# Performance work log

Measured on AMD Instinct MI355X. Metric: run time of the kernel, lower is better.

The kernel has to match this reference:

```python
import jax, jax.numpy as jnp
import numpy as np

DECAY = 0.99
EPS = 1e-5  # Laplace smoothing eps in cluster-size balancing


def _quantize(z_flat, embedding, cluster_size, emb_avg, n_codes):
    # z_flat: [N, D]; embedding: [K, D]
    d = (jnp.sum(z_flat * z_flat, axis=1, keepdims=True)
         + jnp.sum(embedding * embedding, axis=1)
         - 2.0 * (z_flat @ embedding.T))                      # [N, K]
    idx = jnp.argmin(d, axis=1)                               # [N]
    # EMA update (training path). segment_sum == one-hot matmul scatter-add.
    counts = jax.ops.segment_sum(jnp.ones(z_flat.shape[0], z_flat.dtype), idx,
                                 num_segments=n_codes)        # [K]
    new_cs = cluster_size * DECAY + (1.0 - DECAY) * counts
    dw = jax.ops.segment_sum(z_flat, idx, num_segments=n_codes)  # [K, D]
    new_avg = emb_avg * DECAY + (1.0 - DECAY) * dw
    n = new_cs.sum()
    bal = (new_cs + EPS) / (n + n_codes * EPS) * n
    # torch assigns via .data (no autograd) -> stop_gradient for faithfulness
    new_emb = jax.lax.stop_gradient(new_avg / bal[:, None])
    z_q = jnp.take(new_emb, idx, axis=0)  # == one_hot(idx) @ new_emb
    return idx, z_q


def _l2norm(x):
    # F.normalize(x, dim=-1) with eps=1e-12
    return x / jnp.maximum(jnp.linalg.norm(x, axis=-1, keepdims=True), 1e-12)


def reference(z, structure_embedding, style_embedding,
              structure_cluster_size, style_cluster_size,
              structure_embedding_avg, style_embedding_avg):
    b, c, h, w, d = z.shape
    zp = jnp.transpose(z, (0, 2, 3, 4, 1))      # b h w d c
    z_flat = zp.reshape(-1, c)                  # [N, D]
    s_idx, s_q = _quantize(z_flat, structure_embedding, structure_cluster_size,
                           structure_embedding_avg, structure_embedding.shape[0])
    y_idx, y_q = _quantize(z_flat, style_embedding, style_cluster_size,
                           style_embedding_avg, style_embedding.shape[0])

    def back(q):  # [N, C] -> b c h w d
        return jnp.transpose(q.reshape(b, h, w, d, c), (0, 4, 1, 2, 3))

    s_enc = back(s_q)
    y_enc = back(y_q)
    # NOTE: faithful to source — normalize over LAST axis of (b,c,h,w,d),
    # i.e. the spatial depth axis, exactly as F.normalize(dim=-1) does there.
    dis = jnp.mean(jnp.sum(_l2norm(s_enc) * _l2norm(y_enc), axis=-1) ** 2)
    z_q = (s_enc + y_enc) * 0.5
    return z_q, dis, s_idx, y_idx


def setup_inputs() -> dict:
    key = jax.random.key(0)
    k1, k2, k3 = jax.random.split(key, 3)
    B, C, H, W, D = 16, 256, 16, 16, 16
    Ks, Ky = 1024, 512
    return {
        "z": jax.random.normal(k1, (B, C, H, W, D), dtype=jnp.float32),
        "structure_embedding": jax.random.normal(k2, (Ks, C), dtype=jnp.float32),
        "style_embedding": jax.random.normal(k3, (Ky, C), dtype=jnp.float32),
        "structure_cluster_size": jnp.zeros((Ks,), jnp.float32),
        "style_cluster_size": jnp.zeros((Ky,), jnp.float32),
        "structure_embedding_avg": jnp.zeros((Ks, C), jnp.float32),
        "style_embedding_avg": jnp.zeros((Ky, C), jnp.float32),
    }
```

## Files before the change

kernel.cpp:

```cpp
#include <hip/hip_runtime.h>
#include <float.h>

#define NROWS 65536
#define CDIM  256
#define KS    1024
#define KY    512
#define KTOT  1536
#define SPB   4096

#define WB_CNT_S       0
#define WB_CNT_Y       4096
#define WB_RESCUE_CNT  6144
#define WB_DISACC      6152
#define WB_DW_S        6400
#define WB_DW_Y        1054976
#define WB_ZERO_BYTES  1579264
#define WB_EIMG        1579264
#define WB_EN2         2365696
#define WB_IDXS_I      2371840
#define WB_IDXY_I      2633984
#define WB_RLIST_S     2896128
#define WB_RLIST_Y     3158272
#define WB_BASE_S      3420416
#define WB_BASE_Y      3424512
#define WB_CUR_S       3426560
#define WB_CUR_Y       3430656
#define WB_SCALE_S     3432704
#define WB_SCALE_Y     3436800
#define WB_PERM_S      3438848
#define WB_PERM_Y      3700992
#define WB_KSORT_S     3963136
#define WB_KSORT_Y     4225280
#define WB_PS0         4487424
#define WB_PS1         5011712

#define OFF_OUT_ZQ   0
#define OFF_OUT_DIS  16777216
#define OFF_OUT_SIDX 16777217
#define OFF_OUT_YIDX 16842753

typedef __attribute__((ext_vector_type(8)))  _Float16 f16x8;
typedef __attribute__((ext_vector_type(4)))  float    f32x4;

__device__ __forceinline__ unsigned int umn(unsigned int a, unsigned int b) { return a < b ? a : b; }
__device__ __forceinline__ unsigned int umx(unsigned int a, unsigned int b) { return a > b ? a : b; }

__global__ void prep_kernel(const float* __restrict__ Es, const float* __restrict__ Ey,
                            const float* __restrict__ z,
                            unsigned short* __restrict__ eimg, float* __restrict__ en2,
                            float* __restrict__ zf) {
    if (blockIdx.x < 384) {
        int wave = threadIdx.x >> 6, lane = threadIdx.x & 63;
        int k = blockIdx.x * 4 + wave;
        const float* E = (k < KS) ? (Es + (size_t)k * CDIM) : (Ey + (size_t)(k - KS) * CDIM);
        float4 v = *(const float4*)(E + lane * 4);
        float nrm = v.x * v.x + v.y * v.y + v.z * v.z + v.w * v.w;
#pragma unroll
        for (int off = 32; off > 0; off >>= 1) nrm += __shfl_down(nrm, off);
        if (lane == 0) en2[k] = nrm;

        unsigned short q0 = __builtin_bit_cast(unsigned short, (_Float16)v.x);
        unsigned short q1 = __builtin_bit_cast(unsigned short, (_Float16)v.y);
        unsigned short q2 = __builtin_bit_cast(unsigned short, (_Float16)v.z);
        unsigned short q3 = __builtin_bit_cast(unsigned short, (_Float16)v.w);
        uint2 hp = make_uint2((unsigned)q0 | ((unsigned)q1 << 16),
                              (unsigned)q2 | ((unsigned)q3 << 16));
        int c0 = lane * 4;
        int kc = c0 >> 5, g = (c0 >> 3) & 3, j0 = c0 & 7;
        size_t byteoff = (size_t)(k >> 4) * 8192 + (size_t)kc * 1024
                       + (size_t)(g * 16 + (k & 15)) * 16 + (size_t)j0 * 2;
        *(uint2*)((char*)eimg + byteoff) = hp;
    } else {
        __shared__ float Zs[32][257];
        int blk = blockIdx.x - 384;
        int n0 = blk * 32, b = n0 >> 12, s0 = n0 & 4095;
        int t = threadIdx.x;
        const float* zb = z + (size_t)b * CDIM * SPB + s0;
#pragma unroll
        for (int i = 0; i < 32; ++i) {
            int l = i * 256 + t;
            int c = l >> 5, s = l & 31;
            Zs[s][c] = zb[(size_t)c * SPB + s];
        }
        __syncthreads();
#pragma unroll
        for (int j = 0; j < 8; ++j) {
            int gid = j * 256 + t;
            int nl = gid >> 6, fg = gid & 63;
            float4 v = *(const float4*)(&Zs[nl][fg * 4]);
            *(float4*)(&zf[(size_t)(n0 + nl) * 256 + fg * 4]) = v;
        }
    }
}

__device__ __forceinline__ void stage1(const unsigned short* __restrict__ eimg,
                                       int chunk, char* lds, int wave, int lane) {
    const char* gs = (const char*)eimg + (size_t)chunk * 8192 + wave * 2048 + lane * 16;
    char* ls = lds + wave * 2048;
    __builtin_amdgcn_global_load_lds(
        (const __attribute__((address_space(1))) void*)gs,
        (__attribute__((address_space(3))) void*)ls, 16, 0, 0);
    __builtin_amdgcn_global_load_lds(
        (const __attribute__((address_space(1))) void*)(gs + 1024),
        (__attribute__((address_space(3))) void*)(ls + 1024), 16, 0, 0);
}

#define WAITV(n)                                                               \
    asm volatile("s_waitcnt vmcnt(" #n ")");                                   \
    __builtin_amdgcn_sched_barrier(0);

#define PSFLUSH(dst)                                                           \
    {                                                                          \
        _Pragma("unroll")                                                      \
        for (int rg = 0; rg < 2; ++rg)                                         \
        _Pragma("unroll")                                                      \
        for (int q = 0; q < 4; ++q) {                                          \
            unsigned int v1 = m1a[rg][q], v2 = m2a[rg][q];                     \
            _Pragma("unroll")                                                  \
            for (int m = 8; m >= 1; m >>= 1) {                                 \
                unsigned int o1 = (unsigned int)__shfl_xor((int)v1, m);        \
                unsigned int o2 = (unsigned int)__shfl_xor((int)v2, m);        \
                v2 = umn(umn(v2, o2), umx(v1, o1));                            \
                v1 = umn(v1, o1);                                              \
            }                                                                  \
            if ((lane & 15) == 0) {                                            \
                int n = n0 + rg * 16 + (lane >> 4) * 4 + q;                    \
                dst[n] = make_uint2(v1, v2);                                   \
            }                                                                  \
            m1a[rg][q] = 0xFFFFFFFFu; m2a[rg][q] = 0xFFFFFFFFu;                \
        }                                                                      \
    }

#define FLUSHY()                                                               \
    {                                                                          \
        _Pragma("unroll")                                                      \
        for (int rg = 0; rg < 2; ++rg)                                         \
        _Pragma("unroll")                                                      \
        for (int q = 0; q < 4; ++q) {                                          \
            unsigned int v1 = m1a[rg][q], v2 = m2a[rg][q];                     \
            _Pragma("unroll")                                                  \
            for (int m = 8; m >= 1; m >>= 1) {                                 \
                unsigned int o1 = (unsigned int)__shfl_xor((int)v1, m);        \
                unsigned int o2 = (unsigned int)__shfl_xor((int)v2, m);        \
                v2 = umn(umn(v2, o2), umx(v1, o1));                            \
                v1 = umn(v1, o1);                                              \
            }                                                                  \
            if ((lane & 15) == 0) {                                            \
                int kw = (int)(v1 & 0x7FFu) - KS;                              \
                int n = n0 + rg * 16 + (lane >> 4) * 4 + q;                    \
                yidx_f[n] = (float)kw;                                         \
                yidx_i[n] = kw;                                                \
                atomicAdd(&cnt_y[kw], 1);                                      \
                if ((v1 >> 11) + 4 > (v2 >> 11)) {                             \
                    int k2w = (int)(v2 & 0x7FFu) - KS;                         \
                    int pp = atomicAdd(&rescue_cnt[1], 1);                     \
                    if (pp < 65536) rlist_y[pp] = n | (k2w << 16);             \
                }                                                              \
            }                                                                  \
        }                                                                      \
    }

__launch_bounds__(256, 4)
__global__ void assign_kernel(const float* __restrict__ zf, const unsigned short* __restrict__ eimg,
                              const float* __restrict__ en2g,
                              uint2* __restrict__ ps0, uint2* __restrict__ ps1,
                              float* __restrict__ yidx_f, int* __restrict__ yidx_i,
                              int* __restrict__ cnt_y, int* __restrict__ rescue_cnt,
                              int* __restrict__ rlist_y) {
    __shared__ char  sh[4][8192];
    __shared__ float en2l[KTOT];
    const int tid = threadIdx.x, wave = tid >> 6, lane = tid & 63;
    const int half = blockIdx.x & 1;
    const int n0 = (blockIdx.x >> 1) * 128 + wave * 32;
    const int cb = half * 48;

    for (int i = tid; i < KTOT; i += 256) en2l[i] = en2g[i];

    f16x8 A[2][8];
#pragma unroll
    for (int rg = 0; rg < 2; ++rg) {
        const float* zr = zf + (size_t)(n0 + rg * 16 + (lane & 15)) * 256 + (lane >> 4) * 8;
#pragma unroll
        for (int kc = 0; kc < 8; ++kc) {
            float4 f0 = *(const float4*)(zr + kc * 32);
            float4 f1 = *(const float4*)(zr + kc * 32 + 4);
            f16x8 a;
            a[0] = (_Float16)f0.x; a[1] = (_Float16)f0.y;
            a[2] = (_Float16)f0.z; a[3] = (_Float16)f0.w;
            a[4] = (_Float16)f1.x; a[5] = (_Float16)f1.y;
            a[6] = (_Float16)f1.z; a[7] = (_Float16)f1.w;
            A[rg][kc] = a;
        }
    }

    unsigned int m1a[2][4], m2a[2][4];
#pragma unroll
    for (int rg = 0; rg < 2; ++rg)
#pragma unroll
        for (int q = 0; q < 4; ++q) { m1a[rg][q] = 0xFFFFFFFFu; m2a[rg][q] = 0xFFFFFFFFu; }

    stage1(eimg, cb + 0, &sh[0][0], wave, lane);
    stage1(eimg, cb + 1, &sh[1][0], wave, lane);
    stage1(eimg, cb + 2, &sh[2][0], wave, lane);
    __syncthreads();

#pragma unroll 1
    for (int i = 0; i < 48; ++i) {
        if (i < 46)       { WAITV(4); }
        else if (i == 46) { WAITV(2); }
        else              { WAITV(0); }
        __builtin_amdgcn_s_barrier();
        asm volatile("" ::: "memory");
        if (i + 3 < 48) stage1(eimg, cb + i + 3, &sh[(i + 3) & 3][0], wave, lane);

        const int chunk = cb + i;
        const char* bb = &sh[i & 3][0] + lane * 16;
        f32x4 acc0 = {}, acc1 = {};
#pragma unroll
        for (int kc = 0; kc < 8; ++kc) {
            f16x8 B = *(const f16x8*)(bb + kc * 1024);
            acc0 = __builtin_amdgcn_mfma_f32_16x16x32_f16(A[0][kc], B, acc0, 0, 0, 0);
            acc1 = __builtin_amdgcn_mfma_f32_16x16x32_f16(A[1][kc], B, acc1, 0, 0, 0);
        }
        const int kcode = chunk * 16 + (lane & 15);
        const float en0 = en2l[kcode] + 512.0f;
        const unsigned int tag = (unsigned int)kcode;
#pragma unroll
        for (int q = 0; q < 4; ++q) {
            float d0 = fmaf(-2.f, acc0[q], en0);
            unsigned int du0 = (__float_as_uint(d0) & 0xFFFFF800u) | tag;
            m2a[0][q] = umn(m2a[0][q], umx(m1a[0][q], du0));
            m1a[0][q] = umn(m1a[0][q], du0);
            float d1 = fmaf(-2.f, acc1[q], en0);
            unsigned int du1 = (__float_as_uint(d1) & 0xFFFFF800u) | tag;
            m2a[1][q] = umn(m2a[1][q], umx(m1a[1][q], du1));
            m1a[1][q] = umn(m1a[1][q], du1);
        }

        if (half == 1 && i == 15) PSFLUSH(ps1);
    }

    if (half == 0) { PSFLUSH(ps0); }
    else           { FLUSHY(); }
}

__global__ void merge_s_kernel(const uint2* __restrict__ ps0, const uint2* __restrict__ ps1,
                               float* __restrict__ sidx_f, int* __restrict__ sidx_i,
                               int* __restrict__ cnt_s, int* __restrict__ rescue_cnt,
                               int* __restrict__ rlist_s) {
    int n = blockIdx.x * 256 + threadIdx.x;
    uint2 a = ps0[n], b = ps1[n];
    unsigned int v1 = umn(a.x, b.x);
    unsigned int v2 = umn(umn(a.y, b.y), umx(a.x, b.x));
    int kw = (int)(v1 & 0x7FFu);
    sidx_f[n] = (float)kw;
    sidx_i[n] = kw;
    atomicAdd(&cnt_s[kw], 1);
    if ((v1 >> 11) + 4 > (v2 >> 11)) {
        int k2w = (int)(v2 & 0x7FFu);
        int pp = atomicAdd(&rescue_cnt[0], 1);
        if (pp < 65536) rlist_s[pp] = n | (k2w << 16);
    }
}

__global__ void rescue2_kernel(const float* __restrict__ zf,
                               const float* __restrict__ Es, const float* __restrict__ Ey,
                               const float* __restrict__ en2, const int* __restrict__ rcnt,
                               const int* __restrict__ rlist_s, const int* __restrict__ rlist_y,
                               float* __restrict__ sidx_f, float* __restrict__ yidx_f,
                               int* __restrict__ sidx_i, int* __restrict__ yidx_i,
                               int* __restrict__ cnt_s, int* __restrict__ cnt_y) {
    int cs = rcnt[0]; if (cs > 65536) cs = 65536;
    int cy = rcnt[1]; if (cy > 65536) cy = 65536;
    int total = cs + cy;
    const int lane = threadIdx.x & 63;
    const int nw = (gridDim.x * blockDim.x) >> 6;
    for (int e = (int)((blockIdx.x * blockDim.x + threadIdx.x) >> 6); e < total; e += nw) {
        int book = (e >= cs);
        unsigned int ent = (unsigned int)(book ? rlist_y[e - cs] : rlist_s[e]);
        int n  = (int)(ent & 0xFFFFu);
        int k2 = (int)(ent >> 16);
        int* idx_i = book ? yidx_i : sidx_i;
        float* idx_f = book ? yidx_f : sidx_f;
        int* cnt = book ? cnt_y : cnt_s;
        const float* E = book ? Ey : Es;
        const float* en2k = book ? (en2 + KS) : en2;
        int k1 = idx_i[n];
        float4 zv = *(const float4*)(zf + (size_t)n * 256 + lane * 4);
        float4 a  = *(const float4*)(E + (size_t)k1 * 256 + lane * 4);
        float4 c  = *(const float4*)(E + (size_t)k2 * 256 + lane * 4);
        float d1 = zv.x * a.x + zv.y * a.y + zv.z * a.z + zv.w * a.w;
        float d2 = zv.x * c.x + zv.y * c.y + zv.z * c.z + zv.w * c.w;
#pragma unroll
        for (int off = 32; off > 0; off >>= 1) {
            d1 += __shfl_down(d1, off);
            d2 += __shfl_down(d2, off);
        }
        if (lane == 0) {
            float dist1 = en2k[k1] - 2.f * d1;
            float dist2 = en2k[k2] - 2.f * d2;
            int nk = (dist2 < dist1 || (dist2 == dist1 && k2 < k1)) ? k2 : k1;
            if (nk != k1) {
                atomicSub(&cnt[k1], 1);
                atomicAdd(&cnt[nk], 1);
                idx_i[n] = nk;
                idx_f[n] = (float)nk;
            }
        }
    }
}

__global__ void scanbal_kernel(const float* __restrict__ cs_in, const float* __restrict__ cy_in,
                               const int* __restrict__ cnt_s, const int* __restrict__ cnt_y,
                               int* __restrict__ base_s, int* __restrict__ base_y,
                               int* __restrict__ cur_s, int* __restrict__ cur_y,
                               float* __restrict__ scale_s, float* __restrict__ scale_y) {
    __shared__ int   sc[1024];
    __shared__ float sf[1024];
    int K = blockIdx.x ? KY : KS;
    const float* csi = blockIdx.x ? cy_in : cs_in;
    const int*   cnt = blockIdx.x ? cnt_y : cnt_s;
    int* base = blockIdx.x ? base_y : base_s;
    int* cur  = blockIdx.x ? cur_y  : cur_s;
    float* scale = blockIdx.x ? scale_y : scale_s;
    int t = threadIdx.x;
    int c = (t < K) ? cnt[t] : 0;
    float ncs = (t < K) ? (csi[t] * 0.99f + 0.01f * (float)c) : 0.f;
    sc[t] = c;
    __syncthreads();
    for (int off = 1; off < 1024; off <<= 1) {
        int v = sc[t] + ((t >= off) ? sc[t - off] : 0);
        __syncthreads();
        sc[t] = v;
        __syncthreads();
    }
    int incl = sc[t];
    sf[t] = ncs;
    __syncthreads();
    for (int s2 = 512; s2 > 0; s2 >>= 1) {
        if (t < s2) sf[t] += sf[t + s2];
        __syncthreads();
    }
    float nsum = sf[0];
    if (t < K) {
        base[t] = incl - c;
        cur[t]  = incl - c;
        float bal = (ncs + 1e-5f) / (nsum + (float)K * 1e-5f) * nsum;
        scale[t] = 1.0f / bal;
    }
}

__global__ void scatter_kernel(const int* __restrict__ si, const int* __restrict__ yi,
                               int* __restrict__ cur_s, int* __restrict__ cur_y,
                               int* __restrict__ perm_s, int* __restrict__ perm_y,
                               int* __restrict__ ksort_s, int* __restrict__ ksort_y) {
    int i = blockIdx.x * 256 + threadIdx.x;
    if (i < NROWS) {
        int k = si[i]; int p = atomicAdd(&cur_s[k], 1);
        perm_s[p] = i; ksort_s[p] = k;
    } else {
        int n = i - NROWS; int k = yi[n]; int p = atomicAdd(&cur_y[k], 1);
        perm_y[p] = n; ksort_y[p] = k;
    }
}

__global__ void dw_kernel(const float* __restrict__ zf,
                          const int* __restrict__ perm_s, const int* __restrict__ ksort_s,
                          const int* __restrict__ perm_y, const int* __restrict__ ksort_y,
                          float* __restrict__ dw_s, float* __restrict__ dw_y) {
    __shared__ int keys[65];
    __shared__ int rows[64];
    const int t = threadIdx.x;
    int blk = blockIdx.x;
    const int* perm; const int* ks; float* dw; int p0;
    if (blk < NROWS / 64) { perm = perm_s; ks = ksort_s; dw = dw_s; p0 = blk * 64; }
    else                  { perm = perm_y; ks = ksort_y; dw = dw_y; p0 = (blk - NROWS / 64) * 64; }
    if (t < 64) { keys[t] = ks[p0 + t]; rows[t] = perm[p0 + t]; }
    if (t == 64) keys[64] = -1;
    __syncthreads();
    float acc = 0.f;
#pragma unroll 8
    for (int j = 0; j < 64; ++j) {
        acc += zf[(size_t)rows[j] * 256 + t];
        if (keys[j + 1] != keys[j]) {
            atomicAdd(&dw[(size_t)keys[j] * 256 + t], acc);
            acc = 0.f;
        }
    }
}

__global__ void gather_kernel(const float* __restrict__ avg_s, const float* __restrict__ avg_y,
                              const float* __restrict__ dw_s, const float* __restrict__ dw_y,
                              const float* __restrict__ scale_s, const float* __restrict__ scale_y,
                              const int* __restrict__ sidx, const int* __restrict__ yidx,
                              float* __restrict__ zq, float* __restrict__ disacc) {
    __shared__ float qb[256 * 17];
    __shared__ int   si[16], yi[16];
    __shared__ float scs[16], scy[16];
    __shared__ float red[256];
    const int g  = blockIdx.x;
    const int b  = g >> 8;
    const int hw = g & 255;
    const int t  = threadIdx.x;
    if (t < 16) {
        int n = b * SPB + hw * 16 + t;
        int k = sidx[n];
        si[t] = k;
        scs[t] = scale_s[k];
    } else if (t < 32) {
        int n = b * SPB + hw * 16 + (t - 16);
        int k = yidx[n];
        yi[t - 16] = k;
        scy[t - 16] = scale_y[k];
    }
    __syncthreads();
    float ns = 0.f, ny = 0.f, dot = 0.f;
#pragma unroll
    for (int d = 0; d < 16; ++d) {
        size_t so = (size_t)si[d] * CDIM + t;
        size_t yo = (size_t)yi[d] * CDIM + t;
        float s = fmaf(0.01f, dw_s[so], avg_s[so] * 0.99f) * scs[d];
        float y = fmaf(0.01f, dw_y[yo], avg_y[yo] * 0.99f) * scy[d];
        ns  = fmaf(s, s, ns);
        ny  = fmaf(y, y, ny);
        dot = fmaf(s, y, dot);
        qb[t * 17 + d] = 0.5f * (s + y);
    }
    float den = fmaxf(sqrtf(ns), 1e-12f) * fmaxf(sqrtf(ny), 1e-12f);
    float val = dot / den;
    red[t] = val * val;
    __syncthreads();
    for (int s = 128; s > 0; s >>= 1) {
        if (t < s) red[t] += red[t + s];
        __syncthreads();
    }
    if (t == 0) atomicAdd(disacc, red[0]);
    float* zg = zq + (size_t)b * CDIM * SPB + hw * 16;
#pragma unroll
    for (int j = 0; j < 16; ++j) {
        int e = j * 256 + t;
        int c = e >> 4, d = e & 15;
        zg[(size_t)c * SPB + d] = qb[c * 17 + d];
    }
}

__global__ void fin_kernel(const float* __restrict__ disacc, float* __restrict__ out_dis) {
    *out_dis = *disacc * (1.0f / 1048576.0f);
}

extern "C" void kernel_launch(void* const* d_in, const int* in_sizes, int n_in,
                              void* d_out, int out_size, void* d_ws, size_t ws_size,
                              hipStream_t stream) {
    const float* z     = (const float*)d_in[0];
    const float* Es    = (const float*)d_in[1];
    const float* Ey    = (const float*)d_in[2];
    const float* s_cs  = (const float*)d_in[3];
    const float* y_cs  = (const float*)d_in[4];
    const float* s_avg = (const float*)d_in[5];
    const float* y_avg = (const float*)d_in[6];
    float* out = (float*)d_out;
    char*  w   = (char*)d_ws;

    unsigned short* eimg = (unsigned short*)(w + WB_EIMG);
    float* en2    = (float*)(w + WB_EN2);
    int* idxs_i   = (int*)(w + WB_IDXS_I);
    int* idxy_i   = (int*)(w + WB_IDXY_I);
    int* cnt_s    = (int*)(w + WB_CNT_S);
    int* cnt_y    = (int*)(w + WB_CNT_Y);
    int* r_cnt    = (int*)(w + WB_RESCUE_CNT);
    int* rlist_s  = (int*)(w + WB_RLIST_S);
    int* rlist_y  = (int*)(w + WB_RLIST_Y);
    int* base_s   = (int*)(w + WB_BASE_S);
    int* base_y   = (int*)(w + WB_BASE_Y);
    int* cur_s    = (int*)(w + WB_CUR_S);
    int* cur_y    = (int*)(w + WB_CUR_Y);
    float* scale_s = (float*)(w + WB_SCALE_S);
    float* scale_y = (float*)(w + WB_SCALE_Y);
    int* perm_s   = (int*)(w + WB_PERM_S);
    int* perm_y   = (int*)(w + WB_PERM_Y);
    int* ksort_s  = (int*)(w + WB_KSORT_S);
    int* ksort_y  = (int*)(w + WB_KSORT_Y);
    float* dw_s   = (float*)(w + WB_DW_S);
    float* dw_y   = (float*)(w + WB_DW_Y);
    uint2* ps0    = (uint2*)(w + WB_PS0);
    uint2* ps1    = (uint2*)(w + WB_PS1);

    float* zf     = out + OFF_OUT_ZQ;
    float* sidx_f = out + OFF_OUT_SIDX;
    float* yidx_f = out + OFF_OUT_YIDX;

    hipMemsetAsync(w, 0, WB_ZERO_BYTES, stream);

    prep_kernel<<<384 + NROWS / 32, 256, 0, stream>>>(Es, Ey, z, eimg, en2, zf);

    assign_kernel<<<(NROWS / 128) * 2, 256, 0, stream>>>(
        zf, eimg, en2, ps0, ps1, yidx_f, idxy_i, cnt_y, r_cnt, rlist_y);

    merge_s_kernel<<<NROWS / 256, 256, 0, stream>>>(ps0, ps1, sidx_f, idxs_i,
                                                    cnt_s, r_cnt, rlist_s);

    rescue2_kernel<<<512, 256, 0, stream>>>(zf, Es, Ey, en2, r_cnt, rlist_s, rlist_y,
                                            sidx_f, yidx_f, idxs_i, idxy_i, cnt_s, cnt_y);

    scanbal_kernel<<<2, 1024, 0, stream>>>(s_cs, y_cs, cnt_s, cnt_y, base_s, base_y,
                                           cur_s, cur_y, scale_s, scale_y);
    scatter_kernel<<<2 * NROWS / 256, 256, 0, stream>>>(idxs_i, idxy_i, cur_s, cur_y,
                                                        perm_s, perm_y, ksort_s, ksort_y);
    dw_kernel<<<2 * NROWS / 64, 256, 0, stream>>>(zf, perm_s, ksort_s, perm_y, ksort_y, dw_s, dw_y);
    gather_kernel<<<4096, 256, 0, stream>>>(s_avg, y_avg, dw_s, dw_y, scale_s, scale_y,
                                            idxs_i, idxy_i,
                                            out + OFF_OUT_ZQ, (float*)(w + WB_DISACC));
    fin_kernel<<<1, 1, 0, stream>>>((float*)(w + WB_DISACC), out + OFF_OUT_DIS);
}
```

Baseline: 336.5 us.

## Load z directly in assign kernel and co-schedule transpose blocks with it

The z transpose into row-major zf is taken off the critical path before the assign stage. The assign blocks now read their fp16 A fragments straight from the channel-major z tensor with strided loads. The transpose that produces zf (still needed by the later rescue and dw kernels) runs as extra blocks in the same launch, so it overlaps with the MFMA distance search. The trade-off is uncoalesced strided global reads for the A operands and a larger combined LDS footprint per block.

```diff
diff --git a/kernel.cpp b/kernel.cpp
--- a/kernel.cpp
+++ b/kernel.cpp
@@ -45,52 +45,28 @@
 __device__ __forceinline__ unsigned int umn(unsigned int a, unsigned int b) { return a < b ? a : b; }
 __device__ __forceinline__ unsigned int umx(unsigned int a, unsigned int b) { return a > b ? a : b; }
 
-__global__ void prep_kernel(const float* __restrict__ Es, const float* __restrict__ Ey,
-                            const float* __restrict__ z,
-                            unsigned short* __restrict__ eimg, float* __restrict__ en2,
-                            float* __restrict__ zf) {
-    if (blockIdx.x < 384) {
-        int wave = threadIdx.x >> 6, lane = threadIdx.x & 63;
-        int k = blockIdx.x * 4 + wave;
-        const float* E = (k < KS) ? (Es + (size_t)k * CDIM) : (Ey + (size_t)(k - KS) * CDIM);
-        float4 v = *(const float4*)(E + lane * 4);
-        float nrm = v.x * v.x + v.y * v.y + v.z * v.z + v.w * v.w;
-#pragma unroll
-        for (int off = 32; off > 0; off >>= 1) nrm += __shfl_down(nrm, off);
-        if (lane == 0) en2[k] = nrm;
-
-        unsigned short q0 = __builtin_bit_cast(unsigned short, (_Float16)v.x);
-        unsigned short q1 = __builtin_bit_cast(unsigned short, (_Float16)v.y);
-        unsigned short q2 = __builtin_bit_cast(unsigned short, (_Float16)v.z);
-        unsigned short q3 = __builtin_bit_cast(unsigned short, (_Float16)v.w);
-        uint2 hp = make_uint2((unsigned)q0 | ((unsigned)q1 << 16),
-                              (unsigned)q2 | ((unsigned)q3 << 16));
-        int c0 = lane * 4;
-        int kc = c0 >> 5, g = (c0 >> 3) & 3, j0 = c0 & 7;
-        size_t byteoff = (size_t)(k >> 4) * 8192 + (size_t)kc * 1024
-                       + (size_t)(g * 16 + (k & 15)) * 16 + (size_t)j0 * 2;
-        *(uint2*)((char*)eimg + byteoff) = hp;
-    } else {
-        __shared__ float Zs[32][257];
-        int blk = blockIdx.x - 384;
-        int n0 = blk * 32, b = n0 >> 12, s0 = n0 & 4095;
-        int t = threadIdx.x;
-        const float* zb = z + (size_t)b * CDIM * SPB + s0;
-#pragma unroll
-        for (int i = 0; i < 32; ++i) {
-            int l = i * 256 + t;
-            int c = l >> 5, s = l & 31;
-            Zs[s][c] = zb[(size_t)c * SPB + s];
-        }
-        __syncthreads();
-#pragma unroll
-        for (int j = 0; j < 8; ++j) {
-            int gid = j * 256 + t;
-            int nl = gid >> 6, fg = gid & 63;
-            float4 v = *(const float4*)(&Zs[nl][fg * 4]);
-            *(float4*)(&zf[(size_t)(n0 + nl) * 256 + fg * 4]) = v;
-        }
-    }
+__global__ void prep_e(const float* __restrict__ Es, const float* __restrict__ Ey,
+                       unsigned short* __restrict__ eimg, float* __restrict__ en2) {
+    int wave = threadIdx.x >> 6, lane = threadIdx.x & 63;
+    int k = blockIdx.x * 4 + wave;
+    const float* E = (k < KS) ? (Es + (size_t)k * CDIM) : (Ey + (size_t)(k - KS) * CDIM);
+    float4 v = *(const float4*)(E + lane * 4);
+    float nrm = v.x * v.x + v.y * v.y + v.z * v.z + v.w * v.w;
+#pragma unroll
+    for (int off = 32; off > 0; off >>= 1) nrm += __shfl_down(nrm, off);
+    if (lane == 0) en2[k] = nrm;
+
+    unsigned short q0 = __builtin_bit_cast(unsigned short, (_Float16)v.x);
+    unsigned short q1 = __builtin_bit_cast(unsigned short, (_Float16)v.y);
+    unsigned short q2 = __builtin_bit_cast(unsigned short, (_Float16)v.z);
+    unsigned short q3 = __builtin_bit_cast(unsigned short, (_Float16)v.w);
+    uint2 hp = make_uint2((unsigned)q0 | ((unsigned)q1 << 16),
+                          (unsigned)q2 | ((unsigned)q3 << 16));
+    int c0 = lane * 4;
+    int kc = c0 >> 5, g = (c0 >> 3) & 3, j0 = c0 & 7;
+    size_t byteoff = (size_t)(k >> 4) * 8192 + (size_t)kc * 1024
+                   + (size_t)(g * 16 + (k & 15)) * 16 + (size_t)j0 * 2;
+    *(uint2*)((char*)eimg + byteoff) = hp;
 }
 
 __device__ __forceinline__ void stage1(const unsigned short* __restrict__ eimg,
@@ -161,87 +137,111 @@
     }
 
 __launch_bounds__(256, 4)
-__global__ void assign_kernel(const float* __restrict__ zf, const unsigned short* __restrict__ eimg,
-                              const float* __restrict__ en2g,
-                              uint2* __restrict__ ps0, uint2* __restrict__ ps1,
-                              float* __restrict__ yidx_f, int* __restrict__ yidx_i,
-                              int* __restrict__ cnt_y, int* __restrict__ rescue_cnt,
-                              int* __restrict__ rlist_y) {
-    __shared__ char  sh[4][8192];
-    __shared__ float en2l[KTOT];
-    const int tid = threadIdx.x, wave = tid >> 6, lane = tid & 63;
-    const int half = blockIdx.x & 1;
-    const int n0 = (blockIdx.x >> 1) * 128 + wave * 32;
-    const int cb = half * 48;
-
-    for (int i = tid; i < KTOT; i += 256) en2l[i] = en2g[i];
-
-    f16x8 A[2][8];
-#pragma unroll
-    for (int rg = 0; rg < 2; ++rg) {
-        const float* zr = zf + (size_t)(n0 + rg * 16 + (lane & 15)) * 256 + (lane >> 4) * 8;
-#pragma unroll
-        for (int kc = 0; kc < 8; ++kc) {
-            float4 f0 = *(const float4*)(zr + kc * 32);
-            float4 f1 = *(const float4*)(zr + kc * 32 + 4);
-            f16x8 a;
-            a[0] = (_Float16)f0.x; a[1] = (_Float16)f0.y;
-            a[2] = (_Float16)f0.z; a[3] = (_Float16)f0.w;
-            a[4] = (_Float16)f1.x; a[5] = (_Float16)f1.y;
-            a[6] = (_Float16)f1.z; a[7] = (_Float16)f1.w;
-            A[rg][kc] = a;
-        }
-    }
-
-    unsigned int m1a[2][4], m2a[2][4];
-#pragma unroll
-    for (int rg = 0; rg < 2; ++rg)
-#pragma unroll
-        for (int q = 0; q < 4; ++q) { m1a[rg][q] = 0xFFFFFFFFu; m2a[rg][q] = 0xFFFFFFFFu; }
-
-    stage1(eimg, cb + 0, &sh[0][0], wave, lane);
-    stage1(eimg, cb + 1, &sh[1][0], wave, lane);
-    stage1(eimg, cb + 2, &sh[2][0], wave, lane);
-    __syncthreads();
+__global__ void main1_kernel(const float* __restrict__ z, const unsigned short* __restrict__ eimg,
+                             const float* __restrict__ en2g, float* __restrict__ zf,
+                             uint2* __restrict__ ps0, uint2* __restrict__ ps1,
+                             float* __restrict__ yidx_f, int* __restrict__ yidx_i,
+                             int* __restrict__ cnt_y, int* __restrict__ rescue_cnt,
+                             int* __restrict__ rlist_y) {
+    __shared__ char lds_raw[38912];
+
+    if (blockIdx.x < 1024) {
+        char (*sh)[8192] = (char(*)[8192])lds_raw;
+        float* en2l = (float*)(lds_raw + 32768);
+        const int tid = threadIdx.x, wave = tid >> 6, lane = tid & 63;
+        const int half = blockIdx.x & 1;
+        const int n0 = (blockIdx.x >> 1) * 128 + wave * 32;
+        const int cb = half * 48;
+
+        for (int i = tid; i < KTOT; i += 256) en2l[i] = en2g[i];
+
+        const int b = n0 >> 12;
+        const int sb = (n0 & 4095) + (lane & 15);
+        const float* zb = z + (size_t)b * CDIM * SPB;
+        const int g8 = (lane >> 4) * 8;
+        f16x8 A[2][8];
+#pragma unroll
+        for (int rg = 0; rg < 2; ++rg) {
+#pragma unroll
+            for (int kc = 0; kc < 8; ++kc) {
+                f16x8 a;
+#pragma unroll
+                for (int j = 0; j < 8; ++j)
+                    a[j] = (_Float16)zb[(size_t)(g8 + kc * 32 + j) * SPB + sb + rg * 16];
+                A[rg][kc] = a;
+            }
+        }
+
+        unsigned int m1a[2][4], m2a[2][4];
+#pragma unroll
+        for (int rg = 0; rg < 2; ++rg)
+#pragma unroll
+            for (int q = 0; q < 4; ++q) { m1a[rg][q] = 0xFFFFFFFFu; m2a[rg][q] = 0xFFFFFFFFu; }
+
+        stage1(eimg, cb + 0, &sh[0][0], wave, lane);
+        stage1(eimg, cb + 1, &sh[1][0], wave, lane);
+        stage1(eimg, cb + 2, &sh[2][0], wave, lane);
+        __syncthreads();
 
 #pragma unroll 1
-    for (int i = 0; i < 48; ++i) {
-        if (i < 46)       { WAITV(4); }
-        else if (i == 46) { WAITV(2); }
-        else              { WAITV(0); }
-        __builtin_amdgcn_s_barrier();
-        asm volatile("" ::: "memory");
-        if (i + 3 < 48) stage1(eimg, cb + i + 3, &sh[(i + 3) & 3][0], wave, lane);
-
-        const int chunk = cb + i;
-        const char* bb = &sh[i & 3][0] + lane * 16;
-        f32x4 acc0 = {}, acc1 = {};
-#pragma unroll
-        for (int kc = 0; kc < 8; ++kc) {
-            f16x8 B = *(const f16x8*)(bb + kc * 1024);
-            acc0 = __builtin_amdgcn_mfma_f32_16x16x32_f16(A[0][kc], B, acc0, 0, 0, 0);
-            acc1 = __builtin_amdgcn_mfma_f32_16x16x32_f16(A[1][kc], B, acc1, 0, 0, 0);
-        }
-        const int kcode = chunk * 16 + (lane & 15);
-        const float en0 = en2l[kcode] + 512.0f;
-        const unsigned int tag = (unsigned int)kcode;
-#pragma unroll
-        for (int q = 0; q < 4; ++q) {
-            float d0 = fmaf(-2.f, acc0[q], en0);
-            unsigned int du0 = (__float_as_uint(d0) & 0xFFFFF800u) | tag;
-            m2a[0][q] = umn(m2a[0][q], umx(m1a[0][q], du0));
-            m1a[0][q] = umn(m1a[0][q], du0);
-            float d1 = fmaf(-2.f, acc1[q], en0);
-            unsigned int du1 = (__float_as_uint(d1) & 0xFFFFF800u) | tag;
-            m2a[1][q] = umn(m2a[1][q], umx(m1a[1][q], du1));
-            m1a[1][q] = umn(m1a[1][q], du1);
-        }
-
-        if (half == 1 && i == 15) PSFLUSH(ps1);
-    }
-
-    if (half == 0) { PSFLUSH(ps0); }
-    else           { FLUSHY(); }
+        for (int i = 0; i < 48; ++i) {
+            if (i < 46)       { WAITV(4); }
+            else if (i == 46) { WAITV(2); }
+            else              { WAITV(0); }
+            __builtin_amdgcn_s_barrier();
+            asm volatile("" ::: "memory");
+            if (i + 3 < 48) stage1(eimg, cb + i + 3, &sh[(i + 3) & 3][0], wave, lane);
+
+            const int chunk = cb + i;
+            const char* bb = &sh[i & 3][0] + lane * 16;
+            f32x4 acc0 = {}, acc1 = {};
+#pragma unroll
+            for (int kc = 0; kc < 8; ++kc) {
+                f16x8 B = *(const f16x8*)(bb + kc * 1024);
+                acc0 = __builtin_amdgcn_mfma_f32_16x16x32_f16(A[0][kc], B, acc0, 0, 0, 0);
+                acc1 = __builtin_amdgcn_mfma_f32_16x16x32_f16(A[1][kc], B, acc1, 0, 0, 0);
+            }
+            const int kcode = chunk * 16 + (lane & 15);
+            const float en0 = en2l[kcode] + 512.0f;
+            const unsigned int tag = (unsigned int)kcode;
+#pragma unroll
+            for (int q = 0; q < 4; ++q) {
+                float d0 = fmaf(-2.f, acc0[q], en0);
+                unsigned int du0 = (__float_as_uint(d0) & 0xFFFFF800u) | tag;
+                m2a[0][q] = umn(m2a[0][q], umx(m1a[0][q], du0));
+                m1a[0][q] = umn(m1a[0][q], du0);
+                float d1 = fmaf(-2.f, acc1[q], en0);
+                unsigned int du1 = (__float_as_uint(d1) & 0xFFFFF800u) | tag;
+                m2a[1][q] = umn(m2a[1][q], umx(m1a[1][q], du1));
+                m1a[1][q] = umn(m1a[1][q], du1);
+            }
+
+            if (half == 1 && i == 15) PSFLUSH(ps1);
+        }
+
+        if (half == 0) { PSFLUSH(ps0); }
+        else           { FLUSHY(); }
+    } else {
+        float (*Zs)[257] = (float(*)[257])lds_raw;
+        int blk = blockIdx.x - 1024;
+        int n0 = blk * 32, b = n0 >> 12, s0 = n0 & 4095;
+        int t = threadIdx.x;
+        const float* zb = z + (size_t)b * CDIM * SPB + s0;
+#pragma unroll
+        for (int i = 0; i < 32; ++i) {
+            int l = i * 256 + t;
+            int c = l >> 5, s = l & 31;
+            Zs[s][c] = zb[(size_t)c * SPB + s];
+        }
+        __syncthreads();
+#pragma unroll
+        for (int j = 0; j < 8; ++j) {
+            int gid = j * 256 + t;
+            int nl = gid >> 6, fg = gid & 63;
+            float4 v = *(const float4*)(&Zs[nl][fg * 4]);
+            *(float4*)(&zf[(size_t)(n0 + nl) * 256 + fg * 4]) = v;
+        }
+    }
 }
 
 __global__ void merge_s_kernel(const uint2* __restrict__ ps0, const uint2* __restrict__ ps1,
@@ -491,10 +491,10 @@
 
     hipMemsetAsync(w, 0, WB_ZERO_BYTES, stream);
 
-    prep_kernel<<<384 + NROWS / 32, 256, 0, stream>>>(Es, Ey, z, eimg, en2, zf);
-
-    assign_kernel<<<(NROWS / 128) * 2, 256, 0, stream>>>(
-        zf, eimg, en2, ps0, ps1, yidx_f, idxy_i, cnt_y, r_cnt, rlist_y);
+    prep_e<<<384, 256, 0, stream>>>(Es, Ey, eimg, en2);
+
+    main1_kernel<<<1024 + 2048, 256, 0, stream>>>(
+        z, eimg, en2, zf, ps0, ps1, yidx_f, idxy_i, cnt_y, r_cnt, rlist_y);
 
     merge_s_kernel<<<NROWS / 256, 256, 0, stream>>>(ps0, ps1, sidx_f, idxs_i,
                                                     cnt_s, r_cnt, rlist_s);
```

New measurement: 305.1 us. 1.1x faster.
